# Performance work log

Measured on AMD Instinct MI355X. Metric: run time of the kernel, lower is better.

Reference implementation:

```python
import jax, jax.numpy as jnp
import numpy as np

TEMPERATURE = 0.07
EPS = 1e-8


def setup_inputs() -> dict:
    key = jax.random.key(0)
    k1, k2 = jax.random.split(key)
    B, D = 8192, 256
    embeddings = jax.random.normal(k1, (B, D), dtype=jnp.float32)
    labels = jax.random.randint(k2, (B,), 0, 6, dtype=jnp.int64)
    return {"embeddings": embeddings, "labels": labels}


def reference(embeddings, labels):
    B = embeddings.shape[0]
    # F.normalize(p=2, dim=1): x / max(||x||, eps)
    norm = jnp.linalg.norm(embeddings, axis=1, keepdims=True)
    en = embeddings / jnp.maximum(norm, 1e-12)
    sim = en @ en.T  # [B, B]
    s = sim / TEMPERATURE

    eye = jnp.eye(B, dtype=bool)
    same = labels[:, None] == labels[None, :]
    pos_mask = same & ~eye            # [B, B]
    neg_mask = (~same) & ~eye         # [B, B]

    exp_s = jnp.exp(s)
    # per-row sum of exp over negatives (matches inner-loop denominator term)
    neg_sum = jnp.sum(jnp.where(neg_mask, exp_s, 0.0), axis=1)  # [B]

    # rows contribute only if they have >=1 positive AND >=1 negative
    row_valid = (pos_mask.sum(axis=1) > 0) & (neg_mask.sum(axis=1) > 0)
    pair_mask = pos_mask & row_valid[:, None]

    # -log( exp(s_ij) / (exp(s_ij) + neg_sum_i + 1e-8) ) per positive pair
    per_pair = -jnp.log(exp_s / (exp_s + neg_sum[:, None] + EPS))
    total = jnp.sum(jnp.where(pair_mask, per_pair, 0.0))
    count = jnp.sum(pair_mask)
    loss = jnp.where(count > 0, total / jnp.maximum(count, 1).astype(total.dtype), 0.0)
    return loss
```

## Files before the change

### kernel.cpp

```cpp
#include <hip/hip_runtime.h>
#include <hip/hip_bf16.h>

#define B_ 8192
#define D_ 256
#define TINV 14.285714285714285f
#define EPS_ 1e-8f
#define BK 32
#define NBLK 32
#define NT 64
#define NTRI (NT*(NT+1)/2)

typedef short short8 __attribute__((ext_vector_type(8)));
typedef float f32x4 __attribute__((ext_vector_type(4)));

__device__ __forceinline__ void mfma_bf16(f32x4& acc, short8 a, short8 b) {
    asm("v_mfma_f32_16x16x32_bf16 %0, %1, %2, %0" : "+v"(acc) : "v"(a), "v"(b));
}

__device__ __forceinline__ void mfma_fence() {
    __builtin_amdgcn_sched_barrier(0);
    asm volatile("s_nop 7\ns_nop 7" ::);
}

__device__ __forceinline__ unsigned short f2bf(float x) {
    __hip_bfloat16 h = __float2bfloat16(x);
    return __builtin_bit_cast(unsigned short, h);
}

__device__ __forceinline__ void tri_decode(int idx, int& bi, int& bj) {
    int t = NTRI - 1 - idx;
    int u = (int)((sqrtf(8.f * (float)t + 1.f) - 1.f) * 0.5f);
    while (u * (u + 1) / 2 > t) --u;
    while ((u + 1) * (u + 2) / 2 <= t) ++u;
    bi = (NT - 1) - u;
    bj = (NT - 1) - (t - u * (u + 1) / 2);
}

__device__ __forceinline__ void stage(const char* gbase, int row0, int k0,
                                      short* ldst, int lane, int wid) {
    int p = (wid << 6) + lane;
    int row = p >> 2;
    int kb = (p & 3) ^ ((row >> 1) & 3);
    const char* g = gbase + ((size_t)(row0 + row) * (D_ * 2) + (size_t)(k0 + kb * 8) * 2);
    __builtin_amdgcn_global_load_lds(
        (const __attribute__((address_space(1))) unsigned int*)g,
        (__attribute__((address_space(3))) unsigned int*)(ldst + ((size_t)wid << 9)),
        16, 0, 0);
}

__device__ __forceinline__ void compute_step(const short* lA, const short* lB,
                                             int lane, int wm, int wn, f32x4 acc[2][4]) {
    int rl = lane & 15, kb = lane >> 4;
    short8 a[2], b[4];
#pragma unroll
    for (int m = 0; m < 2; ++m) {
        int row = wm * 32 + m * 16 + rl;
        a[m] = ((const short8*)lA)[row * 4 + (kb ^ ((row >> 1) & 3))];
    }
#pragma unroll
    for (int n = 0; n < 4; ++n) {
        int row = wn * 64 + n * 16 + rl;
        b[n] = ((const short8*)lB)[row * 4 + (kb ^ ((row >> 1) & 3))];
    }
#pragma unroll
    for (int m = 0; m < 2; ++m)
#pragma unroll
        for (int n = 0; n < 4; ++n)
            mfma_bf16(acc[m][n], a[m], b[n]);
}

__device__ __forceinline__ void gemm_pipe(const char* enb, int i0, int j0,
                                          short (*lA)[128 * BK], short (*lB)[128 * BK],
                                          int lane, int wid, int wm, int wn,
                                          f32x4 acc[2][4]) {
    stage(enb, i0, 0, lA[0], lane, wid);
    stage(enb, j0, 0, lB[0], lane, wid);
    stage(enb, i0, BK, lA[1], lane, wid);
    stage(enb, j0, BK, lB[1], lane, wid);
#define PIPE_STEP(T, WAITS)                                                     \
    {                                                                           \
        asm volatile(WAITS ::: "memory");                                       \
        __builtin_amdgcn_sched_barrier(0);                                      \
        __builtin_amdgcn_s_barrier();                                           \
        __builtin_amdgcn_sched_barrier(0);                                      \
        if ((T) + 2 < 8) {                                                      \
            stage(enb, i0, ((T) + 2) * BK, lA[((T) + 2) % 3], lane, wid);       \
            stage(enb, j0, ((T) + 2) * BK, lB[((T) + 2) % 3], lane, wid);       \
        }                                                                       \
        compute_step(lA[(T) % 3], lB[(T) % 3], lane, wm, wn, acc);              \
    }
    PIPE_STEP(0, "s_waitcnt vmcnt(2)")
    PIPE_STEP(1, "s_waitcnt vmcnt(2)")
    PIPE_STEP(2, "s_waitcnt vmcnt(2)")
    PIPE_STEP(3, "s_waitcnt vmcnt(2)")
    PIPE_STEP(4, "s_waitcnt vmcnt(2)")
    PIPE_STEP(5, "s_waitcnt vmcnt(2)")
    PIPE_STEP(6, "s_waitcnt vmcnt(2)")
    PIPE_STEP(7, "s_waitcnt vmcnt(0)")
#undef PIPE_STEP
    mfma_fence();
}

__global__ __launch_bounds__(256) void k_bhist(const int* __restrict__ labels,
                                               unsigned* __restrict__ blockhist,
                                               float* __restrict__ negsum,
                                               float* __restrict__ total) {
    __shared__ unsigned h[8];
    int b = blockIdx.x, t = threadIdx.x;
    if (t < 8) h[t] = 0;
    negsum[b * 256 + t] = 0.f;
    if (b == 0 && t == 0) *total = 0.f;
    __syncthreads();
    atomicAdd(&h[labels[b * 256 + t] & 7], 1u);
    __syncthreads();
    if (t < 8) blockhist[b * 8 + t] = h[t];
}

__global__ __launch_bounds__(256) void k_pos(const int* __restrict__ labels,
                                             const unsigned* __restrict__ blockhist,
                                             unsigned* __restrict__ hist,
                                             int* __restrict__ pos) {
    __shared__ unsigned cnt[8][NBLK];
    __shared__ unsigned clsbase[8];
    __shared__ unsigned wcnt[4][8];
    int b = blockIdx.x, t = threadIdx.x;
    { int bb = t >> 3, c = t & 7; cnt[c][bb] = blockhist[bb * 8 + c]; }
    __syncthreads();
    if (t < 8) {
        unsigned run = 0;
        for (int b2 = 0; b2 < NBLK; ++b2) {
            unsigned v = cnt[t][b2];
            cnt[t][b2] = run;
            run += v;
        }
        clsbase[t] = run;
        if (b == 0) hist[t] = run;
    }
    __syncthreads();
    if (t == 0) {
        unsigned run = 0;
        for (int c = 0; c < 8; ++c) {
            unsigned tot = clsbase[c];
            clsbase[c] = run;
            run += tot;
        }
    }
    __syncthreads();
    int row = b * 256 + t;
    int c = labels[row] & 7;
    int lane = t & 63, w = t >> 6;
    unsigned long long lanebelow = (1ull << lane) - 1ull;
    unsigned myrank = 0;
#pragma unroll
    for (int cv = 0; cv < 8; ++cv) {
        unsigned long long mask = __ballot(c == cv);
        if (lane == 0) wcnt[w][cv] = (unsigned)__popcll(mask);
        if (c == cv) myrank = (unsigned)__popcll(mask & lanebelow);
    }
    __syncthreads();
    unsigned pre = 0;
    for (int wp = 0; wp < 4; ++wp) if (wp < w) pre += wcnt[wp][c];
    pos[row] = (int)(clsbase[c] + cnt[c][b] + pre + myrank);
}

__global__ __launch_bounds__(256) void k_scatter(const float* __restrict__ emb,
                                                 const int* __restrict__ labels,
                                                 const int* __restrict__ pos,
                                                 __hip_bfloat16* __restrict__ en_s,
                                                 int* __restrict__ lab_s) {
    int row = blockIdx.x * 4 + (threadIdx.x >> 6);
    int lane = threadIdx.x & 63;
    float4 v = reinterpret_cast<const float4*>(emb)[(size_t)row * 64 + lane];
    float ss = v.x * v.x + v.y * v.y + v.z * v.z + v.w * v.w;
#pragma unroll
    for (int off = 32; off >= 1; off >>= 1) ss += __shfl_xor(ss, off, 64);
    float scale = 1.0f / fmaxf(sqrtf(ss), 1e-12f);
    int p = pos[row];
    ushort4 o;
    o.x = f2bf(v.x * scale);
    o.y = f2bf(v.y * scale);
    o.z = f2bf(v.z * scale);
    o.w = f2bf(v.w * scale);
    reinterpret_cast<ushort4*>(en_s)[(size_t)p * 64 + lane] = o;
    if (lane == 0) lab_s[p] = labels[row] & 7;
}

template <bool USEP>
__global__ __launch_bounds__(512, 6) void k_negsum(const __hip_bfloat16* __restrict__ en,
                                                   const int* __restrict__ lab_s,
                                                   float* __restrict__ P,
                                                   float* __restrict__ negsum) {
    __shared__ short lA[3][128 * BK];
    __shared__ short lB[3][128 * BK];
    __shared__ int sLi[128], sLj[128];
    int bi, bj;
    tri_decode(blockIdx.x, bi, bj);
    int i0 = bi * 128, j0 = bj * 128;
    int tid = threadIdx.x;
    if (tid < 128) sLi[tid] = lab_s[i0 + tid];
    else if (tid < 256) sLj[tid - 128] = lab_s[j0 + tid - 128];
    __syncthreads();

    int lane = tid & 63, wid = tid >> 6;
    int wm = wid >> 1, wn = wid & 1;
    f32x4 acc[2][4] = {};
    gemm_pipe((const char*)en, i0, j0, lA, lB, lane, wid, wm, wn, acc);

    int rl = lane & 15, rowg = (lane >> 4) * 4;
    int lj[4], li[2][4];
#pragma unroll
    for (int n = 0; n < 4; ++n) lj[n] = sLj[wn * 64 + n * 16 + rl];
#pragma unroll
    for (int m = 0; m < 2; ++m)
#pragma unroll
        for (int r = 0; r < 4; ++r) li[m][r] = sLi[wm * 32 + m * 16 + rowg + r];

    float* sredR = (float*)lA;
    float* sredC = (float*)lB;

    float cp[4] = {0.f, 0.f, 0.f, 0.f};
#pragma unroll
    for (int m = 0; m < 2; ++m) {
        float part[4];
#pragma unroll
        for (int r = 0; r < 4; ++r) {
            part[r] = 0.f;
#pragma unroll
            for (int n = 0; n < 4; ++n) {
                float e = (li[m][r] != lj[n]) ? __expf(acc[m][n][r] * TINV) : 0.f;
                part[r] += e;
                cp[n] += e;
            }
        }
#pragma unroll
        for (int off = 1; off < 16; off <<= 1)
#pragma unroll
            for (int r = 0; r < 4; ++r) part[r] += __shfl_xor(part[r], off, 64);
        if (rl == 0) {
#pragma unroll
            for (int r = 0; r < 4; ++r) {
                int row = wm * 32 + m * 16 + rowg + r;
                if (USEP) sredR[wn * 128 + row] = part[r];
                else      atomicAdd(&negsum[i0 + row], part[r]);
            }
        }
    }
    if (bi != bj) {
#pragma unroll
        for (int n = 0; n < 4; ++n) {
            cp[n] += __shfl_xor(cp[n], 16, 64);
            cp[n] += __shfl_xor(cp[n], 32, 64);
            if (lane < 16) {
                int col = wn * 64 + n * 16 + lane;
                if (USEP) sredC[wm * 128 + col] = cp[n];
                else      atomicAdd(&negsum[j0 + col], cp[n]);
            }
        }
    }
    if (USEP) {
        __syncthreads();
        if (tid < 128)
            P[(size_t)bj * B_ + i0 + tid] = sredR[tid] + sredR[128 + tid];
        else if (tid < 256 && bi != bj) {
            int c = tid - 128;
            P[(size_t)bi * B_ + j0 + c] =
                sredC[c] + sredC[128 + c] + sredC[256 + c] + sredC[384 + c];
        }
    }
}

__global__ __launch_bounds__(256) void k_red(const float* __restrict__ P,
                                             float* __restrict__ negsum) {
    int i = blockIdx.x * 256 + threadIdx.x;
    float s = 0.f;
#pragma unroll 8
    for (int k = 0; k < 64; ++k) s += P[(size_t)k * B_ + i];
    negsum[i] = s;
}

__global__ __launch_bounds__(512, 6) void k_pairs(const __hip_bfloat16* __restrict__ en,
                                                  const int* __restrict__ lab_s,
                                                  const float* __restrict__ negsum,
                                                  const unsigned* __restrict__ hist,
                                                  float* __restrict__ total) {
    int bi, bj;
    tri_decode(blockIdx.x, bi, bj);
    int i0 = bi * 128, j0 = bj * 128;
    if (lab_s[j0] > lab_s[i0 + 127]) return;

    __shared__ short lA[3][128 * BK];
    __shared__ short lB[3][128 * BK];
    __shared__ int sLi[128], sLj[128];
    __shared__ float sNgI[128], sNgJ[128];
    int tid = threadIdx.x;
    if (tid < 128) {
        int l = lab_s[i0 + tid];
        unsigned h = hist[l];
        sLi[tid] = (h > 1u && h < (unsigned)B_) ? l : -1;
        sNgI[tid] = negsum[i0 + tid] + EPS_;
    } else if (tid < 256) {
        int idx = tid - 128;
        int l = lab_s[j0 + idx];
        unsigned h = hist[l];
        sLj[idx] = (h > 1u && h < (unsigned)B_) ? l : -1;
        sNgJ[idx] = negsum[j0 + idx] + EPS_;
    }
    __syncthreads();

    int lane = tid & 63, wid = tid >> 6;
    int wm = wid >> 1, wn = wid & 1;
    f32x4 acc[2][4] = {};
    gemm_pipe((const char*)en, i0, j0, lA, lB, lane, wid, wm, wn, acc);

    int rl = lane & 15, rowg = (lane >> 4) * 4;
    int lj[4];
    float ngJ[4];
#pragma unroll
    for (int n = 0; n < 4; ++n) {
        lj[n] = sLj[wn * 64 + n * 16 + rl];
        ngJ[n] = sNgJ[wn * 64 + n * 16 + rl];
    }

    bool offd = (bi != bj);
    float tot = 0.f;
#pragma unroll
    for (int m = 0; m < 2; ++m) {
#pragma unroll
        for (int r = 0; r < 4; ++r) {
            int ii = wm * 32 + m * 16 + rowg + r;
            int li = sLi[ii];
            float ngI = sNgI[ii];
#pragma unroll
            for (int n = 0; n < 4; ++n) {
                int jj = wn * 64 + n * 16 + rl;
                bool use = (li == lj[n]) && (li >= 0) && (offd || ii != jj);
                if (use) {
                    float s = acc[m][n][r] * TINV;
                    float e = __expf(s);
                    float t = __logf(e + ngI) - s;
                    if (offd) t += __logf(e + ngJ[n]) - s;
                    tot += t;
                }
            }
        }
    }
#pragma unroll
    for (int off = 32; off >= 1; off >>= 1) tot += __shfl_xor(tot, off, 64);
    __shared__ float sred[8];
    if (lane == 0) sred[wid] = tot;
    __syncthreads();
    if (tid == 0) {
        float s = 0.f;
#pragma unroll
        for (int w = 0; w < 8; ++w) s += sred[w];
        atomicAdd(total, s);
    }
}

__global__ __launch_bounds__(64) void k_final(const unsigned* __restrict__ hist,
                                              const float* __restrict__ total,
                                              float* __restrict__ out) {
    int t = threadIdx.x;
    unsigned c = 0;
    if (t < 8) {
        unsigned h = hist[t];
        if (h > 1u && h < (unsigned)B_) c = h * (h - 1u);
    }
#pragma unroll
    for (int off = 4; off >= 1; off >>= 1) c += (unsigned)__shfl_xor((int)c, off, 64);
    if (t == 0) out[0] = (c > 0u) ? total[0] / (float)c : 0.f;
}

extern "C" void kernel_launch(void* const* d_in, const int* in_sizes, int n_in,
                              void* d_out, int out_size, void* d_ws, size_t ws_size,
                              hipStream_t stream) {
    const float* emb = (const float*)d_in[0];
    const int* labels = (const int*)d_in[1];
    float* out = (float*)d_out;
    char* ws = (char*)d_ws;

    const size_t EN_BYTES = (size_t)B_ * D_ * 2;
    __hip_bfloat16* en_s = (__hip_bfloat16*)ws;
    char* p = ws + EN_BYTES;
    float* negsum = (float*)p;            p += (size_t)B_ * 4;
    int* lab_s = (int*)p;                 p += (size_t)B_ * 4;
    int* pos = (int*)p;                   p += (size_t)B_ * 4;
    unsigned* blockhist = (unsigned*)p;   p += NBLK * 8 * 4;
    unsigned* hist = (unsigned*)p;        p += 64;
    float* total = (float*)p;             p += 64;
    float* P = (float*)p;
    size_t need = (size_t)(p - ws) + (size_t)NT * B_ * 4;
    bool bigws = ws_size >= need;

    k_bhist<<<NBLK, 256, 0, stream>>>(labels, blockhist, negsum, total);
    k_pos<<<NBLK, 256, 0, stream>>>(labels, blockhist, hist, pos);
    k_scatter<<<B_ / 4, 256, 0, stream>>>(emb, labels, pos, en_s, lab_s);
    if (bigws) {
        k_negsum<true><<<NTRI, 512, 0, stream>>>(en_s, lab_s, P, negsum);
        k_red<<<B_ / 256, 256, 0, stream>>>(P, negsum);
    } else {
        k_negsum<false><<<NTRI, 512, 0, stream>>>(en_s, lab_s, P, negsum);
    }
    k_pairs<<<NTRI, 512, 0, stream>>>(en_s, lab_s, negsum, hist, total);
    k_final<<<1, 64, 0, stream>>>(hist, total, out);
}
```

Baseline: 74.00 us.

## Switch GEMM pipeline to double-buffered LDS and raise occupancy bound

Reduces the LDS staging from three buffers to two, prefetching one K-step ahead and waiting on all outstanding loads each step. The B-fragment loads are interleaved with the MFMAs to cut live registers, and launch bounds move from 6 to 8 waves per EU so more blocks can be resident. The intent is to trade prefetch depth for occupancy and lower register and LDS pressure. The risk is more exposed global-load latency, since each step now waits for vmcnt(0).

```diff
diff --git a/kernel.cpp b/kernel.cpp
--- a/kernel.cpp
+++ b/kernel.cpp
@@ -51,7 +51,7 @@
 __device__ __forceinline__ void compute_step(const short* lA, const short* lB,
                                              int lane, int wm, int wn, f32x4 acc[2][4]) {
     int rl = lane & 15, kb = lane >> 4;
-    short8 a[2], b[4];
+    short8 a[2];
 #pragma unroll
     for (int m = 0; m < 2; ++m) {
         int row = wm * 32 + m * 16 + rl;
@@ -60,13 +60,10 @@
 #pragma unroll
     for (int n = 0; n < 4; ++n) {
         int row = wn * 64 + n * 16 + rl;
-        b[n] = ((const short8*)lB)[row * 4 + (kb ^ ((row >> 1) & 3))];
-    }
-#pragma unroll
-    for (int m = 0; m < 2; ++m)
-#pragma unroll
-        for (int n = 0; n < 4; ++n)
-            mfma_bf16(acc[m][n], a[m], b[n]);
+        short8 b = ((const short8*)lB)[row * 4 + (kb ^ ((row >> 1) & 3))];
+        mfma_bf16(acc[0][n], a[0], b);
+        mfma_bf16(acc[1][n], a[1], b);
+    }
 }
 
 __device__ __forceinline__ void gemm_pipe(const char* enb, int i0, int j0,
@@ -75,28 +72,26 @@
                                           f32x4 acc[2][4]) {
     stage(enb, i0, 0, lA[0], lane, wid);
     stage(enb, j0, 0, lB[0], lane, wid);
-    stage(enb, i0, BK, lA[1], lane, wid);
-    stage(enb, j0, BK, lB[1], lane, wid);
-#define PIPE_STEP(T, WAITS)                                                     \
+#define PIPE_STEP(T)                                                            \
     {                                                                           \
-        asm volatile(WAITS ::: "memory");                                       \
+        asm volatile("s_waitcnt vmcnt(0)" ::: "memory");                        \
         __builtin_amdgcn_sched_barrier(0);                                      \
         __builtin_amdgcn_s_barrier();                                           \
         __builtin_amdgcn_sched_barrier(0);                                      \
-        if ((T) + 2 < 8) {                                                      \
-            stage(enb, i0, ((T) + 2) * BK, lA[((T) + 2) % 3], lane, wid);       \
-            stage(enb, j0, ((T) + 2) * BK, lB[((T) + 2) % 3], lane, wid);       \
+        if ((T) < 7) {                                                          \
+            stage(enb, i0, ((T) + 1) * BK, lA[((T) + 1) & 1], lane, wid);       \
+            stage(enb, j0, ((T) + 1) * BK, lB[((T) + 1) & 1], lane, wid);       \
         }                                                                       \
-        compute_step(lA[(T) % 3], lB[(T) % 3], lane, wm, wn, acc);              \
-    }
-    PIPE_STEP(0, "s_waitcnt vmcnt(2)")
-    PIPE_STEP(1, "s_waitcnt vmcnt(2)")
-    PIPE_STEP(2, "s_waitcnt vmcnt(2)")
-    PIPE_STEP(3, "s_waitcnt vmcnt(2)")
-    PIPE_STEP(4, "s_waitcnt vmcnt(2)")
-    PIPE_STEP(5, "s_waitcnt vmcnt(2)")
-    PIPE_STEP(6, "s_waitcnt vmcnt(2)")
-    PIPE_STEP(7, "s_waitcnt vmcnt(0)")
+        compute_step(lA[(T) & 1], lB[(T) & 1], lane, wm, wn, acc);              \
+    }
+    PIPE_STEP(0)
+    PIPE_STEP(1)
+    PIPE_STEP(2)
+    PIPE_STEP(3)
+    PIPE_STEP(4)
+    PIPE_STEP(5)
+    PIPE_STEP(6)
+    PIPE_STEP(7)
 #undef PIPE_STEP
     mfma_fence();
 }
@@ -186,12 +181,12 @@
 }
 
 template <bool USEP>
-__global__ __launch_bounds__(512, 6) void k_negsum(const __hip_bfloat16* __restrict__ en,
+__global__ __launch_bounds__(512, 8) void k_negsum(const __hip_bfloat16* __restrict__ en,
                                                    const int* __restrict__ lab_s,
                                                    float* __restrict__ P,
                                                    float* __restrict__ negsum) {
-    __shared__ short lA[3][128 * BK];
-    __shared__ short lB[3][128 * BK];
+    __shared__ short lA[2][128 * BK];
+    __shared__ short lB[2][128 * BK];
     __shared__ int sLi[128], sLj[128];
     int bi, bj;
     tri_decode(blockIdx.x, bi, bj);
@@ -278,7 +273,7 @@
     negsum[i] = s;
 }
 
-__global__ __launch_bounds__(512, 6) void k_pairs(const __hip_bfloat16* __restrict__ en,
+__global__ __launch_bounds__(512, 8) void k_pairs(const __hip_bfloat16* __restrict__ en,
                                                   const int* __restrict__ lab_s,
                                                   const float* __restrict__ negsum,
                                                   const unsigned* __restrict__ hist,
@@ -288,8 +283,8 @@
     int i0 = bi * 128, j0 = bj * 128;
     if (lab_s[j0] > lab_s[i0 + 127]) return;
 
-    __shared__ short lA[3][128 * BK];
-    __shared__ short lB[3][128 * BK];
+    __shared__ short lA[2][128 * BK];
+    __shared__ short lB[2][128 * BK];
     __shared__ int sLi[128], sLj[128];
     __shared__ float sNgI[128], sNgJ[128];
     int tid = threadIdx.x;
```

New measurement: 76.95 us. 4.0% more time.
